# Kernel optimization log

Measured on AMD Instinct MI355X. Metric: run time of the kernel, lower is better.

## Reference

```python
import jax, jax.numpy as jnp
import numpy as np

HEADS = 4
DIM_HEAD = 32
SCALE = DIM_HEAD ** -0.5


def setup_inputs() -> dict:
    key = jax.random.key(0)
    k1, k2, k3 = jax.random.split(key, 3)
    B, C, H, W = 4, 128, 64, 64
    inner = HEADS * DIM_HEAD  # 128
    x = jax.random.normal(k1, (B, C, H, W), dtype=jnp.float32)
    # 1x1 conv weights == channel-mixing matrices [out_ch, in_ch]
    w_qkv = jax.random.normal(k2, (inner * 3, C), dtype=jnp.float32) * (C ** -0.5)
    w_proj = jax.random.normal(k3, (C, inner), dtype=jnp.float32) * (inner ** -0.5)
    b_proj = jnp.zeros((C,), dtype=jnp.float32)
    return {"x": x, "w_qkv": w_qkv, "w_proj": w_proj, "b_proj": b_proj}


def reference(x, w_qkv, w_proj, b_proj):
    b, c, h, w = x.shape
    n = h * w
    # 1x1 conv = per-pixel matmul over channels
    qkv = jnp.einsum('bchw,oc->bohw', x, w_qkv)  # [B, 3*inner, H, W]
    q, k, v = jnp.split(qkv, 3, axis=1)

    def to_heads(t):
        # [B, inner, H, W] -> [B, heads, HW, dim_head]
        return t.reshape(b, HEADS, DIM_HEAD, n).transpose(0, 1, 3, 2)

    q = to_heads(q) * SCALE
    k = to_heads(k)
    v = to_heads(v)
    # scores [B, heads, HW, HW]; softmax is max-stabilized (matches torch amax-subtract)
    scores = jnp.einsum('bhnd,bhmd->bhnm', q, k)
    attn = jax.nn.softmax(scores, axis=-1)
    out = jnp.einsum('bhnm,bhmd->bhnd', attn, v)  # [B, heads, HW, dim_head]
    out = out.transpose(0, 1, 3, 2).reshape(b, HEADS * DIM_HEAD, h, w)
    return jnp.einsum('bchw,oc->bohw', out, w_proj) + b_proj[None, :, None, None]
```

## Files before the change

### kernel.cpp

```cpp
#include <hip/hip_runtime.h>

typedef _Float16 f16;
typedef unsigned short u16;
typedef __attribute__((ext_vector_type(8))) f16 f16x8;
typedef __attribute__((ext_vector_type(4))) f16 f16x4;
typedef __attribute__((ext_vector_type(4))) float floatx4;

#define NPIX 4096
#define KT   128
#define NT   (NPIX / KT)
#define VROW 136

__global__ __launch_bounds__(256) void qkv_mfma(
    const float* __restrict__ x, const float* __restrict__ w,
    f16* __restrict__ qh, f16* __restrict__ kh, f16* __restrict__ vth)
{
    __shared__ f16 wlds[64 * 136];
    const int tid  = threadIdx.x;
    const int wave = tid >> 6;
    const int lane = tid & 63;
    const int quad = lane >> 4;
    const int l16  = lane & 15;
    const int pbase = blockIdx.x * 64;
    const int y     = blockIdx.y;
    const int b     = blockIdx.z;

#pragma unroll
    for (int i = 0; i < 8; ++i) {
        int idx = i * 256 + tid;
        int o = idx >> 5, ch = idx & 31;
        float4 wv = *(const float4*)(w + (size_t)(y * 64 + o) * 128 + ch * 4);
        f16x4 h; h[0] = (f16)wv.x; h[1] = (f16)wv.y; h[2] = (f16)wv.z; h[3] = (f16)wv.w;
        *(f16x4*)&wlds[o * 136 + ch * 4] = h;
    }
    __syncthreads();

    const float* xb = x + (size_t)b * 128 * NPIX;
    const int type = y >> 1;

    if (type < 2) {
        const int p_row = pbase + wave * 16 + l16;
        f16x8 af[4];
#pragma unroll
        for (int kc = 0; kc < 4; ++kc) {
            const int c0 = kc * 32 + quad * 8;
#pragma unroll
            for (int j = 0; j < 8; ++j)
                af[kc][j] = (f16)xb[(size_t)(c0 + j) * NPIX + p_row];
        }
        floatx4 acc[4];
#pragma unroll
        for (int n = 0; n < 4; ++n) acc[n] = floatx4{0.f, 0.f, 0.f, 0.f};
#pragma unroll
        for (int n = 0; n < 4; ++n)
#pragma unroll
            for (int kc = 0; kc < 4; ++kc) {
                f16x8 bf = *(const f16x8*)&wlds[(n * 16 + l16) * 136 + kc * 32 + quad * 8];
                acc[n] = __builtin_amdgcn_mfma_f32_16x16x32_f16(af[kc], bf, acc[n], 0, 0, 0);
            }
        const float qs = (type == 0) ? 0.17677669529663687f * 1.4426950408889634f : 1.0f;
        f16* dst = (type == 0) ? qh : kh;
#pragma unroll
        for (int n = 0; n < 4; ++n) {
            const int og   = y * 64 + n * 16 + l16;
            const int head = (og >> 5) & 3;
            const int d    = og & 31;
            f16* base = dst + (size_t)(b * 4 + head) * NPIX * 32;
#pragma unroll
            for (int r = 0; r < 4; ++r) {
                const int p = pbase + wave * 16 + quad * 4 + r;
                base[(size_t)p * 32 + d] = (f16)(acc[n][r] * qs);
            }
        }
    } else {
        const int p_col = pbase + wave * 16 + l16;
        f16x8 bf[4];
#pragma unroll
        for (int kc = 0; kc < 4; ++kc) {
            const int c0 = kc * 32 + quad * 8;
#pragma unroll
            for (int j = 0; j < 8; ++j)
                bf[kc][j] = (f16)xb[(size_t)(c0 + j) * NPIX + p_col];
        }
        floatx4 acc[4];
#pragma unroll
        for (int m = 0; m < 4; ++m) acc[m] = floatx4{0.f, 0.f, 0.f, 0.f};
#pragma unroll
        for (int m = 0; m < 4; ++m)
#pragma unroll
            for (int kc = 0; kc < 4; ++kc) {
                f16x8 af = *(const f16x8*)&wlds[(m * 16 + l16) * 136 + kc * 32 + quad * 8];
                acc[m] = __builtin_amdgcn_mfma_f32_16x16x32_f16(af, bf[kc], acc[m], 0, 0, 0);
            }
#pragma unroll
        for (int m = 0; m < 4; ++m)
#pragma unroll
            for (int r = 0; r < 4; ++r) {
                const int og   = y * 64 + m * 16 + quad * 4 + r;
                const int head = (og >> 5) & 3;
                const int d    = og & 31;
                vth[((size_t)(b * 4 + head) * 32 + d) * NPIX + p_col] = (f16)acc[m][r];
            }
    }
}

#define ATTN_STEP(BUF, KF, KFN, TNXT)                                          \
{                                                                              \
                    \
    if ((TNXT) < NT) {                                                         \
        _Pragma("unroll")                                                      \
        for (int t = 0; t < 8; ++t)                                            \
            KFN[t] = *(const f16x8*)(kp + (size_t)((TNXT) * KT + t * 16) * 32);\
    }                                                                          \
         \
    int4 nv0, nv1;                                                             \
    if ((TNXT) < NT) {                                                         \
        const int4* vs = (const int4*)(vrow + (TNXT) * KT);                    \
        nv0 = vs[vcc]; nv1 = vs[vcc + 1];                                      \
    }                                                                          \
                                        \
    f16x4 vf[8][2];                                                            \
    _Pragma("unroll")                                                          \
    for (int c = 0; c < 8; ++c) {                                              \
        _Pragma("unroll")                                                      \
        for (int dh = 0; dh < 2; ++dh)                                         \
            vf[c][dh] = *(const f16x4*)&vlds[BUF][(dh * 16 + l16) * VROW + c * 16 + quad * 4]; \
    }                                                                          \
                     \
    floatx4 st0[8], st1[8];                                                    \
    _Pragma("unroll")                                                          \
    for (int t = 0; t < 8; ++t) {                                              \
        floatx4 z = {0.f, 0.f, 0.f, 0.f};                                      \
        st0[t] = __builtin_amdgcn_mfma_f32_16x16x32_f16(KF[t], qB[0], z, 0, 0, 0); \
    }                                                                          \
    _Pragma("unroll")                                                          \
    for (int t = 0; t < 8; ++t) {                                              \
        floatx4 z = {0.f, 0.f, 0.f, 0.f};                                      \
        st1[t] = __builtin_amdgcn_mfma_f32_16x16x32_f16(KF[t], qB[1], z, 0, 0, 0); \
    }                                                                          \
                   \
    f16x4 pf0[8], pf1[8];                                                      \
    float ls0 = 0.f, ls1 = 0.f;                                                \
    _Pragma("unroll")                                                          \
    for (int c = 0; c < 8; ++c) {                                              \
        float e0 = __builtin_amdgcn_exp2f(st0[c][0]);                          \
        float e1 = __builtin_amdgcn_exp2f(st0[c][1]);                          \
        float e2 = __builtin_amdgcn_exp2f(st0[c][2]);                          \
        float e3 = __builtin_amdgcn_exp2f(st0[c][3]);                          \
        ls0 += (e0 + e1) + (e2 + e3);                                          \
        pf0[c][0] = (f16)e0; pf0[c][1] = (f16)e1;                              \
        pf0[c][2] = (f16)e2; pf0[c][3] = (f16)e3;                              \
    }                                                                          \
              \
    _Pragma("unroll")                                                          \
    for (int c = 0; c < 8; ++c) {                                              \
        oacc[0][0] = __builtin_amdgcn_mfma_f32_16x16x16f16(pf0[c], vf[c][0], oacc[0][0], 0, 0, 0); \
        oacc[0][1] = __builtin_amdgcn_mfma_f32_16x16x16f16(pf0[c], vf[c][1], oacc[0][1], 0, 0, 0); \
        float e0 = __builtin_amdgcn_exp2f(st1[c][0]);                          \
        float e1 = __builtin_amdgcn_exp2f(st1[c][1]);                          \
        float e2 = __builtin_amdgcn_exp2f(st1[c][2]);                          \
        float e3 = __builtin_amdgcn_exp2f(st1[c][3]);                          \
        ls1 += (e0 + e1) + (e2 + e3);                                          \
        pf1[c][0] = (f16)e0; pf1[c][1] = (f16)e1;                              \
        pf1[c][2] = (f16)e2; pf1[c][3] = (f16)e3;                              \
    }                                                                          \
    lsum[0] += ls0; lsum[1] += ls1;                                            \
    _Pragma("unroll")                                                          \
    for (int c = 0; c < 8; ++c) {                                              \
        oacc[1][0] = __builtin_amdgcn_mfma_f32_16x16x16f16(pf1[c], vf[c][0], oacc[1][0], 0, 0, 0); \
        oacc[1][1] = __builtin_amdgcn_mfma_f32_16x16x16f16(pf1[c], vf[c][1], oacc[1][1], 0, 0, 0); \
    }                                                                          \
    \
    if ((TNXT) < NT) {                                                         \
        *(int4*)&vlds[(BUF) ^ 1][voff]     = nv0;                              \
        *(int4*)&vlds[(BUF) ^ 1][voff + 8] = nv1;                              \
    }                                                                          \
    __syncthreads();                                                           \
}

__global__ __launch_bounds__(256, 2) void attn_kernel(
    const f16* __restrict__ qh, const f16* __restrict__ kh,
    const f16* __restrict__ vth, f16* __restrict__ att)
{
    __shared__ f16 vlds[2][32 * VROW];

    const int tid  = threadIdx.x;
    const int wave = tid >> 6;
    const int lane = tid & 63;
    const int quad = lane >> 4;
    const int l16  = lane & 15;
    const int bh   = blockIdx.y;
    const int qbase = blockIdx.x * 128 + wave * 32;

    const f16* kb = kh + (size_t)bh * NPIX * 32;
    const f16* vb = vth + (size_t)bh * 32 * NPIX;
    const f16* kp = kb + (size_t)l16 * 32 + quad * 8;

    const int vr = tid >> 3, vcc = (tid & 7) * 2;
    const int voff = vr * VROW + vcc * 8;
    const f16* vrow = vb + (size_t)vr * NPIX;

    f16x8 qB[2];
#pragma unroll
    for (int h = 0; h < 2; ++h)
        qB[h] = *(const f16x8*)(qh + ((size_t)bh * NPIX + qbase + h * 16 + l16) * 32 + quad * 8);

    floatx4 oacc[2][2];
#pragma unroll
    for (int h = 0; h < 2; ++h)
#pragma unroll
        for (int dh = 0; dh < 2; ++dh) oacc[h][dh] = floatx4{0.f, 0.f, 0.f, 0.f};
    float lsum[2] = {0.f, 0.f};

    f16x8 kfA[8], kfB[8];
    {
        const int4* vs = (const int4*)vrow;
        int4 a = vs[vcc], b2 = vs[vcc + 1];
        *(int4*)&vlds[0][voff]     = a;
        *(int4*)&vlds[0][voff + 8] = b2;
    }
#pragma unroll
    for (int t = 0; t < 8; ++t)
        kfA[t] = *(const f16x8*)(kp + (size_t)(t * 16) * 32);
    __syncthreads();

    for (int it = 0; it < NT / 2; ++it) {
        const int t0 = it * 2;
        ATTN_STEP(0, kfA, kfB, t0 + 1);
        ATTN_STEP(1, kfB, kfA, t0 + 2);
    }

#pragma unroll
    for (int h = 0; h < 2; ++h) {
        float l = lsum[h];
        l += __shfl_xor(l, 16);
        l += __shfl_xor(l, 32);
        const float inv = 1.0f / l;
#pragma unroll
        for (int r = 0; r < 4; ++r) {
            const float invr = __shfl(inv, quad * 4 + r);
            const int q = qbase + h * 16 + quad * 4 + r;
            f16* ob = att + ((size_t)bh * NPIX + q) * 32;
            ob[l16]      = (f16)(oacc[h][0][r] * invr);
            ob[16 + l16] = (f16)(oacc[h][1][r] * invr);
        }
    }
}

__global__ __launch_bounds__(256) void proj_mfma(
    const f16* __restrict__ att, const float* __restrict__ wp,
    const float* __restrict__ bp, float* __restrict__ out)
{
    __shared__ f16 wplds[128 * 136];
    __shared__ float bplds[128];
    const int tid  = threadIdx.x;
    const int wave = tid >> 6;
    const int lane = tid & 63;
    const int quad = lane >> 4;
    const int l16  = lane & 15;
    const int pbase = blockIdx.x * 64;
    const int b     = blockIdx.y;

    if (tid < 128) bplds[tid] = bp[tid];
#pragma unroll
    for (int i = 0; i < 16; ++i) {
        int idx = i * 256 + tid;
        int o = idx >> 5, ch = idx & 31;
        float4 wv = *(const float4*)(wp + (size_t)o * 128 + ch * 4);
        f16x4 h; h[0] = (f16)wv.x; h[1] = (f16)wv.y; h[2] = (f16)wv.z; h[3] = (f16)wv.w;
        *(f16x4*)&wplds[o * 136 + ch * 4] = h;
    }
    __syncthreads();

    const f16* ab = att + (size_t)b * 4 * NPIX * 32;
    const int p_col = pbase + wave * 16 + l16;
    f16x8 bf[4];
#pragma unroll
    for (int kc = 0; kc < 4; ++kc)
        bf[kc] = *(const f16x8*)(ab + ((size_t)kc * NPIX + p_col) * 32 + quad * 8);

    floatx4 acc[8];
#pragma unroll
    for (int m = 0; m < 8; ++m) acc[m] = floatx4{0.f, 0.f, 0.f, 0.f};
#pragma unroll
    for (int m = 0; m < 8; ++m)
#pragma unroll
        for (int kc = 0; kc < 4; ++kc) {
            f16x8 af = *(const f16x8*)&wplds[(m * 16 + l16) * 136 + kc * 32 + quad * 8];
            acc[m] = __builtin_amdgcn_mfma_f32_16x16x32_f16(af, bf[kc], acc[m], 0, 0, 0);
        }

#pragma unroll
    for (int m = 0; m < 8; ++m)
#pragma unroll
        for (int r = 0; r < 4; ++r) {
            const int o = m * 16 + quad * 4 + r;
            out[((size_t)b * 128 + o) * NPIX + p_col] = acc[m][r] + bplds[o];
        }
}

extern "C" void kernel_launch(void* const* d_in, const int* in_sizes, int n_in,
                              void* d_out, int out_size, void* d_ws, size_t ws_size,
                              hipStream_t stream)
{
    const float* x      = (const float*)d_in[0];
    const float* w_qkv  = (const float*)d_in[1];
    const float* w_proj = (const float*)d_in[2];
    const float* b_proj = (const float*)d_in[3];
    float* out = (float*)d_out;

    char* ws = (char*)d_ws;
    f16* qh  = (f16*)(ws);
    f16* kh  = (f16*)(ws + (4u << 20));
    f16* vth = (f16*)(ws + (8u << 20));
    f16* att = (f16*)(ws + (12u << 20));

    qkv_mfma<<<dim3(64, 6, 4), 256, 0, stream>>>(x, w_qkv, qh, kh, vth);
    attn_kernel<<<dim3(32, 16, 1), 256, 0, stream>>>(qh, kh, vth, att);
    proj_mfma<<<dim3(64, 4, 1), 256, 0, stream>>>(att, w_proj, b_proj, out);
}
```

Measured before the change: 127.2 us.

## Store V pre-swizzled into MFMA fragment layout and drop LDS staging

The QKV kernel now writes V directly in the per-lane MFMA B-fragment order, using the same compute path as Q/K. The attention kernel then loads V fragments straight from global memory with one 8-byte load per fragment. This removes the LDS double buffer, the shared-memory stores and the per-tile __syncthreads. The cost is that every wave reads V from global/L2 on its own rather than sharing one staged copy per block, and those loads sit in the inner loop without explicit prefetch.

```diff
diff --git a/kernel.cpp b/kernel.cpp
--- a/kernel.cpp
+++ b/kernel.cpp
@@ -9,11 +9,11 @@
 #define NPIX 4096
 #define KT   128
 #define NT   (NPIX / KT)
-#define VROW 136
+#define VBH  131072
 
 __global__ __launch_bounds__(256) void qkv_mfma(
     const float* __restrict__ x, const float* __restrict__ w,
-    f16* __restrict__ qh, f16* __restrict__ kh, f16* __restrict__ vth)
+    f16* __restrict__ qh, f16* __restrict__ kh, f16* __restrict__ vfrag)
 {
     __shared__ f16 wlds[64 * 136];
     const int tid  = threadIdx.x;
@@ -38,26 +38,27 @@
     const float* xb = x + (size_t)b * 128 * NPIX;
     const int type = y >> 1;
 
+    const int p_row = pbase + wave * 16 + l16;
+    f16x8 af[4];
+#pragma unroll
+    for (int kc = 0; kc < 4; ++kc) {
+        const int c0 = kc * 32 + quad * 8;
+#pragma unroll
+        for (int j = 0; j < 8; ++j)
+            af[kc][j] = (f16)xb[(size_t)(c0 + j) * NPIX + p_row];
+    }
+    floatx4 acc[4];
+#pragma unroll
+    for (int n = 0; n < 4; ++n) acc[n] = floatx4{0.f, 0.f, 0.f, 0.f};
+#pragma unroll
+    for (int n = 0; n < 4; ++n)
+#pragma unroll
+        for (int kc = 0; kc < 4; ++kc) {
+            f16x8 bf = *(const f16x8*)&wlds[(n * 16 + l16) * 136 + kc * 32 + quad * 8];
+            acc[n] = __builtin_amdgcn_mfma_f32_16x16x32_f16(af[kc], bf, acc[n], 0, 0, 0);
+        }
+
     if (type < 2) {
-        const int p_row = pbase + wave * 16 + l16;
-        f16x8 af[4];
-#pragma unroll
-        for (int kc = 0; kc < 4; ++kc) {
-            const int c0 = kc * 32 + quad * 8;
-#pragma unroll
-            for (int j = 0; j < 8; ++j)
-                af[kc][j] = (f16)xb[(size_t)(c0 + j) * NPIX + p_row];
-        }
-        floatx4 acc[4];
-#pragma unroll
-        for (int n = 0; n < 4; ++n) acc[n] = floatx4{0.f, 0.f, 0.f, 0.f};
-#pragma unroll
-        for (int n = 0; n < 4; ++n)
-#pragma unroll
-            for (int kc = 0; kc < 4; ++kc) {
-                f16x8 bf = *(const f16x8*)&wlds[(n * 16 + l16) * 136 + kc * 32 + quad * 8];
-                acc[n] = __builtin_amdgcn_mfma_f32_16x16x32_f16(af[kc], bf, acc[n], 0, 0, 0);
-            }
         const float qs = (type == 0) ? 0.17677669529663687f * 1.4426950408889634f : 1.0f;
         f16* dst = (type == 0) ? qh : kh;
 #pragma unroll
@@ -73,60 +74,39 @@
             }
         }
     } else {
-        const int p_col = pbase + wave * 16 + l16;
-        f16x8 bf[4];
-#pragma unroll
-        for (int kc = 0; kc < 4; ++kc) {
-            const int c0 = kc * 32 + quad * 8;
-#pragma unroll
-            for (int j = 0; j < 8; ++j)
-                bf[kc][j] = (f16)xb[(size_t)(c0 + j) * NPIX + p_col];
-        }
-        floatx4 acc[4];
-#pragma unroll
-        for (int m = 0; m < 4; ++m) acc[m] = floatx4{0.f, 0.f, 0.f, 0.f};
-#pragma unroll
-        for (int m = 0; m < 4; ++m)
-#pragma unroll
-            for (int kc = 0; kc < 4; ++kc) {
-                f16x8 af = *(const f16x8*)&wlds[(m * 16 + l16) * 136 + kc * 32 + quad * 8];
-                acc[m] = __builtin_amdgcn_mfma_f32_16x16x32_f16(af, bf[kc], acc[m], 0, 0, 0);
-            }
-#pragma unroll
-        for (int m = 0; m < 4; ++m)
-#pragma unroll
-            for (int r = 0; r < 4; ++r) {
-                const int og   = y * 64 + m * 16 + quad * 4 + r;
-                const int head = (og >> 5) & 3;
-                const int d    = og & 31;
-                vth[((size_t)(b * 4 + head) * 32 + d) * NPIX + p_col] = (f16)acc[m][r];
-            }
-    }
-}
-
-#define ATTN_STEP(BUF, KF, KFN, TNXT)                                          \
+        const int pq = pbase + wave * 16;
+        const int kt = pq >> 7, c = (pq >> 4) & 7;
+#pragma unroll
+        for (int n = 0; n < 4; ++n) {
+            const int head = (y - 4) * 2 + (n >> 1);
+            const int bh_n = b * 4 + head;
+            const size_t off = (size_t)bh_n * VBH + (size_t)kt * 4096 + c * 512
+                             + (n & 1) * 256 + quad * 64 + l16 * 4;
+            f16x4 hv;
+#pragma unroll
+            for (int r = 0; r < 4; ++r) hv[r] = (f16)acc[n][r];
+            *(f16x4*)(vfrag + off) = hv;
+        }
+    }
+}
+
+#define ATTN_STEP(KF, KFN, T, TNXT)                                            \
 {                                                                              \
+        \
+    f16x4 vf[8][2];                                                            \
+    _Pragma("unroll")                                                          \
+    for (int c = 0; c < 8; ++c) {                                              \
+        _Pragma("unroll")                                                      \
+        for (int dh = 0; dh < 2; ++dh)                                         \
+            vf[c][dh] = *(const f16x4*)(vp + (size_t)(T) * 4096 + c * 512 + dh * 256); \
+    }                                                                          \
                     \
     if ((TNXT) < NT) {                                                         \
         _Pragma("unroll")                                                      \
         for (int t = 0; t < 8; ++t)                                            \
             KFN[t] = *(const f16x8*)(kp + (size_t)((TNXT) * KT + t * 16) * 32);\
     }                                                                          \
-         \
-    int4 nv0, nv1;                                                             \
-    if ((TNXT) < NT) {                                                         \
-        const int4* vs = (const int4*)(vrow + (TNXT) * KT);                    \
-        nv0 = vs[vcc]; nv1 = vs[vcc + 1];                                      \
-    }                                                                          \
-                                        \
-    f16x4 vf[8][2];                                                            \
-    _Pragma("unroll")                                                          \
-    for (int c = 0; c < 8; ++c) {                                              \
-        _Pragma("unroll")                                                      \
-        for (int dh = 0; dh < 2; ++dh)                                         \
-            vf[c][dh] = *(const f16x4*)&vlds[BUF][(dh * 16 + l16) * VROW + c * 16 + quad * 4]; \
-    }                                                                          \
-                     \
+                           \
     floatx4 st0[8], st1[8];                                                    \
     _Pragma("unroll")                                                          \
     for (int t = 0; t < 8; ++t) {                                              \
@@ -170,20 +150,12 @@
         oacc[1][0] = __builtin_amdgcn_mfma_f32_16x16x16f16(pf1[c], vf[c][0], oacc[1][0], 0, 0, 0); \
         oacc[1][1] = __builtin_amdgcn_mfma_f32_16x16x16f16(pf1[c], vf[c][1], oacc[1][1], 0, 0, 0); \
     }                                                                          \
-    \
-    if ((TNXT) < NT) {                                                         \
-        *(int4*)&vlds[(BUF) ^ 1][voff]     = nv0;                              \
-        *(int4*)&vlds[(BUF) ^ 1][voff + 8] = nv1;                              \
-    }                                                                          \
-    __syncthreads();                                                           \
 }
 
 __global__ __launch_bounds__(256, 2) void attn_kernel(
     const f16* __restrict__ qh, const f16* __restrict__ kh,
-    const f16* __restrict__ vth, f16* __restrict__ att)
-{
-    __shared__ f16 vlds[2][32 * VROW];
-
+    const f16* __restrict__ vfrag, f16* __restrict__ att)
+{
     const int tid  = threadIdx.x;
     const int wave = tid >> 6;
     const int lane = tid & 63;
@@ -192,13 +164,8 @@
     const int bh   = blockIdx.y;
     const int qbase = blockIdx.x * 128 + wave * 32;
 
-    const f16* kb = kh + (size_t)bh * NPIX * 32;
-    const f16* vb = vth + (size_t)bh * 32 * NPIX;
-    const f16* kp = kb + (size_t)l16 * 32 + quad * 8;
-
-    const int vr = tid >> 3, vcc = (tid & 7) * 2;
-    const int voff = vr * VROW + vcc * 8;
-    const f16* vrow = vb + (size_t)vr * NPIX;
+    const f16* kp = kh + (size_t)bh * NPIX * 32 + (size_t)l16 * 32 + quad * 8;
+    const f16* vp = vfrag + (size_t)bh * VBH + (size_t)lane * 4;
 
     f16x8 qB[2];
 #pragma unroll
@@ -213,21 +180,14 @@
     float lsum[2] = {0.f, 0.f};
 
     f16x8 kfA[8], kfB[8];
-    {
-        const int4* vs = (const int4*)vrow;
-        int4 a = vs[vcc], b2 = vs[vcc + 1];
-        *(int4*)&vlds[0][voff]     = a;
-        *(int4*)&vlds[0][voff + 8] = b2;
-    }
 #pragma unroll
     for (int t = 0; t < 8; ++t)
         kfA[t] = *(const f16x8*)(kp + (size_t)(t * 16) * 32);
-    __syncthreads();
 
     for (int it = 0; it < NT / 2; ++it) {
         const int t0 = it * 2;
-        ATTN_STEP(0, kfA, kfB, t0 + 1);
-        ATTN_STEP(1, kfB, kfA, t0 + 2);
+        ATTN_STEP(kfA, kfB, t0,     t0 + 1);
+        ATTN_STEP(kfB, kfA, t0 + 1, t0 + 2);
     }
 
 #pragma unroll
@@ -310,12 +270,12 @@
     float* out = (float*)d_out;
 
     char* ws = (char*)d_ws;
-    f16* qh  = (f16*)(ws);
-    f16* kh  = (f16*)(ws + (4u << 20));
-    f16* vth = (f16*)(ws + (8u << 20));
-    f16* att = (f16*)(ws + (12u << 20));
-
-    qkv_mfma<<<dim3(64, 6, 4), 256, 0, stream>>>(x, w_qkv, qh, kh, vth);
-    attn_kernel<<<dim3(32, 16, 1), 256, 0, stream>>>(qh, kh, vth, att);
+    f16* qh    = (f16*)(ws);
+    f16* kh    = (f16*)(ws + (4u << 20));
+    f16* vfrag = (f16*)(ws + (8u << 20));
+    f16* att   = (f16*)(ws + (12u << 20));
+
+    qkv_mfma<<<dim3(64, 6, 4), 256, 0, stream>>>(x, w_qkv, qh, kh, vfrag);
+    attn_kernel<<<dim3(32, 16, 1), 256, 0, stream>>>(qh, kh, vfrag, att);
     proj_mfma<<<dim3(64, 4, 1), 256, 0, stream>>>(att, w_proj, b_proj, out);
 }
```

Result: slower. 146.0 us (+14.8%).
